# Kernel tuning notes

Measured on AMD Instinct MI355X. Metric: run time of the kernel, lower is better.

The kernel has to match this reference:

```python
import jax, jax.numpy as jnp
import numpy as np

N_HEADS = 16
D_MODEL = 1024
HEAD_DIM = D_MODEL // N_HEADS
MASK_FILL = -1e8  # matches torch masked_fill value -100000000.0


def setup_inputs() -> dict:
    key = jax.random.key(0)
    ks = jax.random.split(key, 12)
    B, L, P = 2, 2048, 2048
    s = 1.0 / np.sqrt(D_MODEL).astype(np.float32)
    inp = {
        "q": jax.random.normal(ks[0], (B, L, D_MODEL), dtype=jnp.float32),
        "k": jax.random.normal(ks[1], (B, P, D_MODEL), dtype=jnp.float32),
        "v": jax.random.normal(ks[2], (B, P, D_MODEL), dtype=jnp.float32),
        "attention_mask": jnp.ones((B, P), dtype=bool),
        "Wq": jax.random.normal(ks[3], (D_MODEL, D_MODEL), dtype=jnp.float32) * s,
        "bq": jnp.zeros((D_MODEL,), dtype=jnp.float32),
        "Wk": jax.random.normal(ks[4], (D_MODEL, D_MODEL), dtype=jnp.float32) * s,
        "bk": jnp.zeros((D_MODEL,), dtype=jnp.float32),
        "Wv": jax.random.normal(ks[5], (D_MODEL, D_MODEL), dtype=jnp.float32) * s,
        "bv": jnp.zeros((D_MODEL,), dtype=jnp.float32),
        "Wo": jax.random.normal(ks[6], (D_MODEL, D_MODEL), dtype=jnp.float32) * s,
        "bo": jnp.zeros((D_MODEL,), dtype=jnp.float32),
    }
    return inp


def _split_heads(x):
    # [B, S, D] -> [B, n, S, h]
    B, S, _ = x.shape
    return x.reshape(B, S, N_HEADS, HEAD_DIM).transpose(0, 2, 1, 3)


def reference(q, k, v, attention_mask, Wq, bq, Wk, bk, Wv, bv, Wo, bo):
    # Linear projections (torch Linear: x @ W.T + b)
    qm = _split_heads(q @ Wq.T + bq)
    km = _split_heads(k @ Wk.T + bk)
    vm = _split_heads(v @ Wv.T + bv)
    # scores: [B, n, L, P]
    scores = jnp.einsum('bnlh,bnph->bnlp', qm, km) / np.sqrt(HEAD_DIM).astype(np.float32)
    # mask [B, P] -> [B, 1, 1, P]; fill False positions with -1e8 (as in torch source)
    mask = attention_mask[:, None, None, :]
    scores = jnp.where(mask, scores, MASK_FILL)
    attn = jax.nn.softmax(scores, axis=-1)
    # dropout is identity in eval mode
    out = jnp.einsum('bnlp,bnph->bnlh', attn, vm)
    B, _, L, _ = out.shape
    out = out.transpose(0, 2, 1, 3).reshape(B, L, D_MODEL)
    return out @ Wo.T + bo
```

## Files before the change

kernel.cpp:

```cpp
#include <hip/hip_runtime.h>
#include <hip/hip_bf16.h>

typedef __attribute__((ext_vector_type(8))) __bf16 bf16x8;
typedef __attribute__((ext_vector_type(4))) float f32x4;
typedef __attribute__((ext_vector_type(16))) float f32x16;
typedef __attribute__((ext_vector_type(4))) unsigned short u16x4;
typedef __attribute__((ext_vector_type(2))) unsigned int u32x2;

#define LOG2E 1.4426950408889634f
#define FIXED_MAX 32.0f

__device__ __forceinline__ unsigned short f2bf(float f) {
  union { float f; unsigned int u; } x;
  x.f = f;
  unsigned int u = x.u;
  u += 0x7fffu + ((u >> 16) & 1u);
  return (unsigned short)(u >> 16);
}

__device__ __forceinline__ float fexp2(float x) {
  float r;
  asm("v_exp_f32 %0, %1" : "=v"(r) : "v"(x));
  return r;
}

__device__ __forceinline__ unsigned int cvtpk_bf16(float lo, float hi) {
  unsigned int r;
  asm("v_cvt_pk_bf16_f32 %0, %1, %2" : "=v"(r) : "v"(lo), "v"(hi));
  return r;
}

__device__ __forceinline__ void plswap(unsigned int& a, unsigned int& b) {
  auto r = __builtin_amdgcn_permlane32_swap((int)a, (int)b, false, false);
  a = (unsigned int)r[0];
  b = (unsigned int)r[1];
}

__device__ __forceinline__ void gload_lds16(const void* gsrc, void* lds) {
  __builtin_amdgcn_global_load_lds(
      (const __attribute__((address_space(1))) unsigned int*)gsrc,
      (__attribute__((address_space(3))) unsigned int*)lds, 16, 0, 0);
}

__global__ __launch_bounds__(256) void cvt_all(
    const float* __restrict__ q, const float* __restrict__ k, const float* __restrict__ v,
    const float* __restrict__ w0, const float* __restrict__ w1,
    const float* __restrict__ w2, const float* __restrict__ w3,
    unsigned short* __restrict__ qb, unsigned short* __restrict__ kb,
    unsigned short* __restrict__ vb, unsigned short* __restrict__ w0b,
    unsigned short* __restrict__ w1b, unsigned short* __restrict__ w2b,
    unsigned short* __restrict__ w3b) {
  long idx = (long)blockIdx.x * 256 + threadIdx.x;
  const long QV = 1024L * 1024;
  const long WQ = 256L * 1024;
  const float* src;
  unsigned short* dst;
  long base;
  if (idx < QV)                { src = q;  dst = qb;  base = idx; }
  else if (idx < 2 * QV)       { src = k;  dst = kb;  base = idx - QV; }
  else if (idx < 3 * QV)       { src = v;  dst = vb;  base = idx - 2 * QV; }
  else if (idx < 3 * QV + WQ)  { src = w0; dst = w0b; base = idx - 3 * QV; }
  else if (idx < 3 * QV + 2*WQ){ src = w1; dst = w1b; base = idx - 3 * QV - WQ; }
  else if (idx < 3 * QV + 3*WQ){ src = w2; dst = w2b; base = idx - 3 * QV - 2 * WQ; }
  else                         { src = w3; dst = w3b; base = idx - 3 * QV - 3 * WQ; }
  f32x4 val = *(const f32x4*)(src + base * 4);
  u16x4 o;
#pragma unroll
  for (int i = 0; i < 4; ++i) o[i] = f2bf(val[i]);
  *(u16x4*)(dst + base * 4) = o;
}

template <int MODE>
__global__ __launch_bounds__(256) void gemm_bt(
    const unsigned short* A0, const unsigned short* A1, const unsigned short* A2,
    const unsigned short* W0, const unsigned short* W1, const unsigned short* W2,
    const float* b0, const float* b1, const float* b2,
    void* o0, void* o1, void* o2) {
  __shared__ char smem[32768];
  constexpr int BM = (MODE == 1) ? 64 : 128;
  constexpr int NF = (MODE == 1) ? 2 : 4;
  const int z = blockIdx.z;
  const unsigned short* __restrict__ A = (z == 0) ? A0 : (z == 1) ? A1 : A2;
  const unsigned short* __restrict__ W = (z == 0) ? W0 : (z == 1) ? W1 : W2;
  const float* __restrict__ bias = (z == 0) ? b0 : (z == 1) ? b1 : b2;
  void* __restrict__ out = (z == 0) ? o0 : (z == 1) ? o1 : o2;
  const float oscale = (MODE == 0 && z == 0) ? 0.125f * LOG2E : 1.0f;

  const int tid = threadIdx.x;
  const int lane = tid & 63;
  const int wave = tid >> 6;
  const int wm = (MODE == 1) ? 0 : (wave >> 1) * 64;
  const int wn = (MODE == 1) ? wave * 32 : (wave & 1) * 64;
  const int bm0 = blockIdx.x * BM;
  const int bn0 = blockIdx.y * 128;
  const int K = 1024;
  const int srow = tid >> 2;
  const int sg = tid & 3;

  f32x4 acc[4][NF] = {};

  auto stageA = [&](int kt, int buf) {
    char* dst = smem + buf * 8192;
#pragma unroll
    for (int h = 0; h < BM / 64; ++h) {
      int row = srow + h * 64;
      int gs = sg ^ ((row >> 1) & 3);
      gload_lds16((const char*)(A + (long)(bm0 + row) * K + kt * 32) + gs * 16,
                  dst + h * 4096 + tid * 16);
    }
  };
  auto stageB = [&](int kt, int buf) {
    char* dst = smem + 16384 + buf * 8192;
#pragma unroll
    for (int h = 0; h < 2; ++h) {
      int row = srow + h * 64;
      int gs = sg ^ ((row >> 1) & 3);
      gload_lds16((const char*)(W + (long)(bn0 + row) * K + kt * 32) + gs * 16,
                  dst + h * 4096 + tid * 16);
    }
  };

  stageA(0, 0);
  stageB(0, 0);
  __syncthreads();

  const int nk = K / 32;
  for (int kt = 0; kt < nk; ++kt) {
    const int cur = kt & 1;
    if (kt + 1 < nk) { stageA(kt + 1, cur ^ 1); stageB(kt + 1, cur ^ 1); }
    char* curA = smem + cur * 8192;
    char* curB = smem + 16384 + cur * 8192;
    const int kb = (lane >> 4) * 16;
    bf16x8 af[4], bfr[NF];
#pragma unroll
    for (int i = 0; i < 4; ++i) {
      int row = wm + i * 16 + (lane & 15);
      af[i] = *(const bf16x8*)(curA + row * 64 + (kb ^ (((row >> 1) & 3) << 4)));
    }
#pragma unroll
    for (int j = 0; j < NF; ++j) {
      int row = wn + j * 16 + (lane & 15);
      bfr[j] = *(const bf16x8*)(curB + row * 64 + (kb ^ (((row >> 1) & 3) << 4)));
    }
#pragma unroll
    for (int i = 0; i < 4; ++i)
#pragma unroll
      for (int j = 0; j < NF; ++j)
        acc[i][j] = __builtin_amdgcn_mfma_f32_16x16x32_bf16(af[i], bfr[j], acc[i][j], 0, 0, 0);
    __syncthreads();
  }

#pragma unroll
  for (int i = 0; i < 4; ++i) {
#pragma unroll
    for (int j = 0; j < NF; ++j) {
#pragma unroll
      for (int r = 0; r < 4; ++r) {
        int row = bm0 + wm + i * 16 + (lane >> 4) * 4 + r;
        int col = bn0 + wn + j * 16 + (lane & 15);
        float vv = (acc[i][j][r] + bias[col]) * oscale;
        if (MODE == 0) {
          int bb = row >> 11, ll = row & 2047;
          int hh = col >> 6, hd = col & 63;
          long idx;
          if (z == 1) {
            idx = ((((long)((bb * 16 + hh) * 32 + (ll >> 6))) * 8 + (hd >> 3)) * 64
                   + (ll & 63)) * 8 + (hd & 7);
          } else if (z == 2) {
            idx = ((((long)((bb * 16 + hh) * 32 + (ll >> 6))) * 8 + ((ll >> 3) & 7)) * 64
                   + hd) * 8 + (ll & 7);
          } else {
            idx = (((long)(bb * 16 + hh) * 2048 + ll) << 6) + hd;
          }
          ((unsigned short*)out)[idx] = f2bf(vv);
        } else {
          ((float*)out)[(long)row * 1024 + col] = vv;
        }
      }
    }
  }
}

__global__ __launch_bounds__(256, 4) void attn_fwd(
    const unsigned short* __restrict__ Qm,
    const unsigned short* __restrict__ Kblk,
    const unsigned short* __restrict__ Vblk,
    const int* __restrict__ mask,
    unsigned short* __restrict__ ao) {
  __shared__ char smem[37504];
  char* const Kl = smem;
  char* const Vl = smem + 16384;
  unsigned short* const maskb = (unsigned short*)(smem + 32768);
  float* const lsums = (float*)(smem + 36864);
  int* const allm = (int*)(smem + 37376);

  const int tid = threadIdx.x, lane = tid & 63, wave = tid >> 6;
  const int kv = wave & 1;
  const int qg = wave >> 1;
  const int h2 = lane >> 5;
  const int ql = lane & 31;
  const int orig = blockIdx.y * 32 + blockIdx.x;
  const int wgid = (orig & 7) * 128 + (orig >> 3);
  const int bh = wgid >> 5, b = bh >> 4, hh = bh & 15;
  const int q0 = (wgid & 31) * 64;
  const unsigned short* Qbase = Qm + ((long)bh * 2048 + q0 + qg * 32) * 64;
  const char* Kg = (const char*)(Kblk + (long)bh * 2048 * 64);
  const char* Vg = (const char*)(Vblk + (long)bh * 2048 * 64);

  auto stage_pair = [&](int s) {
#pragma unroll
    for (int c = 0; c < 4; ++c) {
      int off = (c * 256 + tid) * 16;
      gload_lds16(Kg + (long)s * 16384 + off, Kl + off);
      gload_lds16(Vg + (long)s * 16384 + off, Vl + off);
    }
  };

  stage_pair(0);

  {
    const int* mrow = mask + b * 2048;
    int p8 = tid * 8;
    int ok = 1;
#pragma unroll
    for (int i = 0; i < 4; ++i) {
      int m0 = mrow[p8 + 2 * i];
      int m1 = mrow[p8 + 2 * i + 1];
      ok &= (m0 != 0) & (m1 != 0);
      unsigned int lo = m0 ? 0u : 1u;
      unsigned int hi = m1 ? 0u : 1u;
      *(unsigned int*)(maskb + p8 + 2 * i) = lo | (hi << 16);
    }
    unsigned long long bal = __ballot(ok != 0);
    if (lane < 8) allm[wave * 8 + lane] = (int)(((bal >> (lane * 8)) & 0xFFull) == 0xFFull);
  }

  bf16x8 qf[4];
#pragma unroll
  for (int ks = 0; ks < 4; ++ks)
    qf[ks] = *(const bf16x8*)(Qbase + (long)ql * 64 + ks * 16 + h2 * 8);

  f32x16 o0 = {}, o1 = {};
  float lsum = 0.f;
  const char* const Kc = Kl + kv * 8192;
  const char* const Vc = Vl + kv * 8192;
  __syncthreads();

  for (int s = 0; s < 16; ++s) {
    const int pt = 2 * s + kv;

    f32x16 s0 = {}, s1 = {};
#pragma unroll
    for (int ks = 0; ks < 4; ++ks) {
      int gl = ks * 2 + h2;
      bf16x8 k0 = *(const bf16x8*)(Kc + gl * 1024 + ql * 16);
      bf16x8 k1 = *(const bf16x8*)(Kc + gl * 1024 + 512 + ql * 16);
      s0 = __builtin_amdgcn_mfma_f32_32x32x16_bf16(k0, qf[ks], s0, 0, 0, 0);
      s1 = __builtin_amdgcn_mfma_f32_32x32x16_bf16(k1, qf[ks], s1, 0, 0, 0);
    }

    if (!allm[pt]) {
#pragma unroll
      for (int rq = 0; rq < 4; ++rq) {
        u16x4 m0 = *(const u16x4*)(maskb + pt * 64 + rq * 8 + 4 * h2);
        u16x4 m1 = *(const u16x4*)(maskb + pt * 64 + 32 + rq * 8 + 4 * h2);
#pragma unroll
        for (int i = 0; i < 4; ++i) {
          s0[rq * 4 + i] = m0[i] ? -1.0e8f : s0[rq * 4 + i];
          s1[rq * 4 + i] = m1[i] ? -1.0e8f : s1[rq * 4 + i];
        }
      }
    }

#pragma unroll
    for (int i = 0; i < 16; ++i) {
      float p = fexp2(s0[i] - FIXED_MAX);
      s0[i] = p; lsum += p;
    }
#pragma unroll
    for (int i = 0; i < 16; ++i) {
      float p = fexp2(s1[i] - FIXED_MAX);
      s1[i] = p; lsum += p;
    }

    bf16x8 pa[4];
    {
      union { unsigned int w[4]; bf16x8 v; } u;
      unsigned int w0, w1, w2, w3;
      w0 = cvtpk_bf16(s0[0],  s0[1]);  w1 = cvtpk_bf16(s0[2],  s0[3]);
      w2 = cvtpk_bf16(s0[4],  s0[5]);  w3 = cvtpk_bf16(s0[6],  s0[7]);
      plswap(w0, w2); plswap(w1, w3);
      u.w[0] = w0; u.w[1] = w1; u.w[2] = w2; u.w[3] = w3; pa[0] = u.v;
      w0 = cvtpk_bf16(s0[8],  s0[9]);  w1 = cvtpk_bf16(s0[10], s0[11]);
      w2 = cvtpk_bf16(s0[12], s0[13]); w3 = cvtpk_bf16(s0[14], s0[15]);
      plswap(w0, w2); plswap(w1, w3);
      u.w[0] = w0; u.w[1] = w1; u.w[2] = w2; u.w[3] = w3; pa[1] = u.v;
      w0 = cvtpk_bf16(s1[0],  s1[1]);  w1 = cvtpk_bf16(s1[2],  s1[3]);
      w2 = cvtpk_bf16(s1[4],  s1[5]);  w3 = cvtpk_bf16(s1[6],  s1[7]);
      plswap(w0, w2); plswap(w1, w3);
      u.w[0] = w0; u.w[1] = w1; u.w[2] = w2; u.w[3] = w3; pa[2] = u.v;
      w0 = cvtpk_bf16(s1[8],  s1[9]);  w1 = cvtpk_bf16(s1[10], s1[11]);
      w2 = cvtpk_bf16(s1[12], s1[13]); w3 = cvtpk_bf16(s1[14], s1[15]);
      plswap(w0, w2); plswap(w1, w3);
      u.w[0] = w0; u.w[1] = w1; u.w[2] = w2; u.w[3] = w3; pa[3] = u.v;
    }

#pragma unroll
    for (int kb = 0; kb < 4; ++kb) {
      int gl = kb * 2 + h2;
      bf16x8 v0 = *(const bf16x8*)(Vc + gl * 1024 + ql * 16);
      bf16x8 v1 = *(const bf16x8*)(Vc + gl * 1024 + 512 + ql * 16);
      o0 = __builtin_amdgcn_mfma_f32_32x32x16_bf16(v0, pa[kb], o0, 0, 0, 0);
      o1 = __builtin_amdgcn_mfma_f32_32x32x16_bf16(v1, pa[kb], o1, 0, 0, 0);
    }

    __syncthreads();
    if (s + 1 < 16) {
      stage_pair(s + 1);
      __syncthreads();
    }
  }

  float lf = lsum + __shfl_xor(lsum, 32);
  if (kv == 1) {
    char* Oc = smem + qg * 16384;
#pragma unroll
    for (int rq = 0; rq < 4; ++rq) {
      f32x4 w0 = {o0[rq*4+0], o0[rq*4+1], o0[rq*4+2], o0[rq*4+3]};
      int d4 = (rq * 8 + 4 * h2) * 4;
      *(f32x4*)(Oc + ql * 256 + (d4 ^ ((ql & 7) << 5))) = w0;
      f32x4 w1 = {o1[rq*4+0], o1[rq*4+1], o1[rq*4+2], o1[rq*4+3]};
      int d41 = 128 + d4;
      *(f32x4*)(Oc + ql * 256 + (d41 ^ ((ql & 7) << 5))) = w1;
    }
    if (h2 == 0) lsums[qg * 64 + ql] = lf;
  }
  __syncthreads();
  if (kv == 0) {
    const char* Oc = smem + qg * 16384;
#pragma unroll
    for (int rq = 0; rq < 4; ++rq) {
      int d4 = (rq * 8 + 4 * h2) * 4;
      f32x4 w0 = *(const f32x4*)(Oc + ql * 256 + (d4 ^ ((ql & 7) << 5)));
      f32x4 w1 = *(const f32x4*)(Oc + ql * 256 + ((128 + d4) ^ ((ql & 7) << 5)));
#pragma unroll
      for (int i = 0; i < 4; ++i) { o0[rq*4+i] += w0[i]; o1[rq*4+i] += w1[i]; }
    }
    lf += lsums[qg * 64 + ql];
    float inv = 1.0f / lf;
    unsigned short* aop = ao + ((long)(b * 2048 + q0 + qg * 32 + ql) << 10) + hh * 64;
#pragma unroll
    for (int rq = 0; rq < 4; ++rq) {
      unsigned int lo = cvtpk_bf16(o0[rq * 4 + 0] * inv, o0[rq * 4 + 1] * inv);
      unsigned int hi = cvtpk_bf16(o0[rq * 4 + 2] * inv, o0[rq * 4 + 3] * inv);
      u32x2 st = {lo, hi};
      *(u32x2*)(aop + rq * 8 + 4 * h2) = st;
    }
#pragma unroll
    for (int rq = 0; rq < 4; ++rq) {
      unsigned int lo = cvtpk_bf16(o1[rq * 4 + 0] * inv, o1[rq * 4 + 1] * inv);
      unsigned int hi = cvtpk_bf16(o1[rq * 4 + 2] * inv, o1[rq * 4 + 3] * inv);
      u32x2 st = {lo, hi};
      *(u32x2*)(aop + 32 + rq * 8 + 4 * h2) = st;
    }
  }
}

extern "C" void kernel_launch(void* const* d_in, const int* in_sizes, int n_in,
                              void* d_out, int out_size, void* d_ws, size_t ws_size,
                              hipStream_t stream) {
  const float* q = (const float*)d_in[0];
  const float* k = (const float*)d_in[1];
  const float* v = (const float*)d_in[2];
  const int* mask = (const int*)d_in[3];
  const float* Wq = (const float*)d_in[4];
  const float* bq = (const float*)d_in[5];
  const float* Wk = (const float*)d_in[6];
  const float* bk = (const float*)d_in[7];
  const float* Wv = (const float*)d_in[8];
  const float* bv = (const float*)d_in[9];
  const float* Wo = (const float*)d_in[10];
  const float* bo = (const float*)d_in[11];

  char* ws = (char*)d_ws;
  unsigned short* qb  = (unsigned short*)(ws + (0L << 20));
  unsigned short* kb  = (unsigned short*)(ws + (8L << 20));
  unsigned short* vb  = (unsigned short*)(ws + (16L << 20));
  unsigned short* wqb = (unsigned short*)(ws + (24L << 20));
  unsigned short* wkb = (unsigned short*)(ws + (26L << 20));
  unsigned short* wvb = (unsigned short*)(ws + (28L << 20));
  unsigned short* wob = (unsigned short*)(ws + (30L << 20));
  unsigned short* Qh  = (unsigned short*)(ws + (32L << 20));
  unsigned short* Kb  = (unsigned short*)(ws + (40L << 20));
  unsigned short* Vb  = (unsigned short*)(ws + (56L << 20));
  unsigned short* aob = (unsigned short*)(ws + (64L << 20));

  cvt_all<<<16384, 256, 0, stream>>>(q, k, v, Wq, Wk, Wv, Wo,
                                     qb, kb, vb, wqb, wkb, wvb, wob);
  gemm_bt<0><<<dim3(32, 8, 3), 256, 0, stream>>>(qb, kb, vb, wqb, wkb, wvb,
                                                 bq, bk, bv, Qh, Kb, Vb);
  attn_fwd<<<dim3(32, 32), 256, 0, stream>>>(Qh, Kb, Vb, mask, aob);
  gemm_bt<1><<<dim3(64, 8, 1), 256, 0, stream>>>(aob, aob, aob, wob, wob, wob,
                                                 bo, bo, bo, d_out, d_out, d_out);
  (void)in_sizes; (void)n_in; (void)out_size; (void)ws_size;
}
```

Measured before the change: 126.7 us.

## Fuse fp32-to-bf16 activation conversion into QKV projection GEMM loads

Activations q, k and v are no longer converted to bf16 in a separate pass. The QKV GEMM now streams fp32 tiles straight into LDS with an 8-way XOR swizzle and packs them to bf16 in registers just before the MFMA. This removes a full read and write of three 8 MB fp32 tensors plus the bf16 re-read. The cost is doubled LDS footprint for the A tile (48 KB shared), which may lower occupancy, and more LDS read traffic and conversion instructions inside the inner loop.

```diff
diff --git a/kernel.cpp b/kernel.cpp
--- a/kernel.cpp
+++ b/kernel.cpp
@@ -30,6 +30,15 @@
   return r;
 }
 
+__device__ __forceinline__ bf16x8 pack8(f32x4 a, f32x4 b) {
+  union { unsigned int w[4]; bf16x8 v; } u;
+  u.w[0] = cvtpk_bf16(a[0], a[1]);
+  u.w[1] = cvtpk_bf16(a[2], a[3]);
+  u.w[2] = cvtpk_bf16(b[0], b[1]);
+  u.w[3] = cvtpk_bf16(b[2], b[3]);
+  return u.v;
+}
+
 __device__ __forceinline__ void plswap(unsigned int& a, unsigned int& b) {
   auto r = __builtin_amdgcn_permlane32_swap((int)a, (int)b, false, false);
   a = (unsigned int)r[0];
@@ -42,27 +51,20 @@
       (__attribute__((address_space(3))) unsigned int*)lds, 16, 0, 0);
 }
 
-__global__ __launch_bounds__(256) void cvt_all(
-    const float* __restrict__ q, const float* __restrict__ k, const float* __restrict__ v,
+__global__ __launch_bounds__(256) void cvt_w(
     const float* __restrict__ w0, const float* __restrict__ w1,
     const float* __restrict__ w2, const float* __restrict__ w3,
-    unsigned short* __restrict__ qb, unsigned short* __restrict__ kb,
-    unsigned short* __restrict__ vb, unsigned short* __restrict__ w0b,
-    unsigned short* __restrict__ w1b, unsigned short* __restrict__ w2b,
-    unsigned short* __restrict__ w3b) {
+    unsigned short* __restrict__ w0b, unsigned short* __restrict__ w1b,
+    unsigned short* __restrict__ w2b, unsigned short* __restrict__ w3b) {
   long idx = (long)blockIdx.x * 256 + threadIdx.x;
-  const long QV = 1024L * 1024;
   const long WQ = 256L * 1024;
   const float* src;
   unsigned short* dst;
   long base;
-  if (idx < QV)                { src = q;  dst = qb;  base = idx; }
-  else if (idx < 2 * QV)       { src = k;  dst = kb;  base = idx - QV; }
-  else if (idx < 3 * QV)       { src = v;  dst = vb;  base = idx - 2 * QV; }
-  else if (idx < 3 * QV + WQ)  { src = w0; dst = w0b; base = idx - 3 * QV; }
-  else if (idx < 3 * QV + 2*WQ){ src = w1; dst = w1b; base = idx - 3 * QV - WQ; }
-  else if (idx < 3 * QV + 3*WQ){ src = w2; dst = w2b; base = idx - 3 * QV - 2 * WQ; }
-  else                         { src = w3; dst = w3b; base = idx - 3 * QV - 3 * WQ; }
+  if (idx < WQ)            { src = w0; dst = w0b; base = idx; }
+  else if (idx < 2 * WQ)   { src = w1; dst = w1b; base = idx - WQ; }
+  else if (idx < 3 * WQ)   { src = w2; dst = w2b; base = idx - 2 * WQ; }
+  else                     { src = w3; dst = w3b; base = idx - 3 * WQ; }
   f32x4 val = *(const f32x4*)(src + base * 4);
   u16x4 o;
 #pragma unroll
@@ -72,15 +74,18 @@
 
 template <int MODE>
 __global__ __launch_bounds__(256) void gemm_bt(
-    const unsigned short* A0, const unsigned short* A1, const unsigned short* A2,
+    const void* A0v, const void* A1v, const void* A2v,
     const unsigned short* W0, const unsigned short* W1, const unsigned short* W2,
     const float* b0, const float* b1, const float* b2,
     void* o0, void* o1, void* o2) {
-  __shared__ char smem[32768];
   constexpr int BM = (MODE == 1) ? 64 : 128;
   constexpr int NF = (MODE == 1) ? 2 : 4;
+  constexpr int ABUF = (MODE == 0) ? 16384 : 8192;
+  constexpr int BBASE = (MODE == 0) ? 32768 : 16384;
+  __shared__ char smem[(MODE == 0) ? 49152 : 32768];
   const int z = blockIdx.z;
-  const unsigned short* __restrict__ A = (z == 0) ? A0 : (z == 1) ? A1 : A2;
+  const char* __restrict__ A =
+      (const char*)((z == 0) ? A0v : (z == 1) ? A1v : A2v);
   const unsigned short* __restrict__ W = (z == 0) ? W0 : (z == 1) ? W1 : W2;
   const float* __restrict__ bias = (z == 0) ? b0 : (z == 1) ? b1 : b2;
   void* __restrict__ out = (z == 0) ? o0 : (z == 1) ? o1 : o2;
@@ -100,17 +105,25 @@
   f32x4 acc[4][NF] = {};
 
   auto stageA = [&](int kt, int buf) {
-    char* dst = smem + buf * 8192;
-#pragma unroll
-    for (int h = 0; h < BM / 64; ++h) {
-      int row = srow + h * 64;
+    char* dst = smem + buf * ABUF;
+    if constexpr (MODE == 0) {
+#pragma unroll
+      for (int c = 0; c < 4; ++c) {
+        int slot = c * 256 + tid;
+        int row = slot >> 3, g = slot & 7;
+        int gs = g ^ (row & 7);
+        gload_lds16(A + ((long)(bm0 + row) * K + kt * 32) * 4 + gs * 16,
+                    dst + slot * 16);
+      }
+    } else {
+      int row = srow;
       int gs = sg ^ ((row >> 1) & 3);
-      gload_lds16((const char*)(A + (long)(bm0 + row) * K + kt * 32) + gs * 16,
-                  dst + h * 4096 + tid * 16);
+      gload_lds16(A + ((long)(bm0 + row) * K + kt * 32) * 2 + gs * 16,
+                  dst + tid * 16);
     }
   };
   auto stageB = [&](int kt, int buf) {
-    char* dst = smem + 16384 + buf * 8192;
+    char* dst = smem + BBASE + buf * 8192;
 #pragma unroll
     for (int h = 0; h < 2; ++h) {
       int row = srow + h * 64;
@@ -128,14 +141,26 @@
   for (int kt = 0; kt < nk; ++kt) {
     const int cur = kt & 1;
     if (kt + 1 < nk) { stageA(kt + 1, cur ^ 1); stageB(kt + 1, cur ^ 1); }
-    char* curA = smem + cur * 8192;
-    char* curB = smem + 16384 + cur * 8192;
+    char* curA = smem + cur * ABUF;
+    char* curB = smem + BBASE + cur * 8192;
     const int kb = (lane >> 4) * 16;
     bf16x8 af[4], bfr[NF];
-#pragma unroll
-    for (int i = 0; i < 4; ++i) {
-      int row = wm + i * 16 + (lane & 15);
-      af[i] = *(const bf16x8*)(curA + row * 64 + (kb ^ (((row >> 1) & 3) << 4)));
+    if constexpr (MODE == 0) {
+      const int j0 = (lane >> 4) * 2;
+#pragma unroll
+      for (int i = 0; i < 4; ++i) {
+        int row = wm + i * 16 + (lane & 15);
+        const char* base = curA + row * 128;
+        f32x4 a0 = *(const f32x4*)(base + ((j0 ^ (row & 7)) << 4));
+        f32x4 a1 = *(const f32x4*)(base + (((j0 + 1) ^ (row & 7)) << 4));
+        af[i] = pack8(a0, a1);
+      }
+    } else {
+#pragma unroll
+      for (int i = 0; i < 4; ++i) {
+        int row = wm + i * 16 + (lane & 15);
+        af[i] = *(const bf16x8*)(curA + row * 64 + (kb ^ (((row >> 1) & 3) << 4)));
+      }
     }
 #pragma unroll
     for (int j = 0; j < NF; ++j) {
@@ -383,9 +408,6 @@
   const float* bo = (const float*)d_in[11];
 
   char* ws = (char*)d_ws;
-  unsigned short* qb  = (unsigned short*)(ws + (0L << 20));
-  unsigned short* kb  = (unsigned short*)(ws + (8L << 20));
-  unsigned short* vb  = (unsigned short*)(ws + (16L << 20));
   unsigned short* wqb = (unsigned short*)(ws + (24L << 20));
   unsigned short* wkb = (unsigned short*)(ws + (26L << 20));
   unsigned short* wvb = (unsigned short*)(ws + (28L << 20));
@@ -395,9 +417,8 @@
   unsigned short* Vb  = (unsigned short*)(ws + (56L << 20));
   unsigned short* aob = (unsigned short*)(ws + (64L << 20));
 
-  cvt_all<<<16384, 256, 0, stream>>>(q, k, v, Wq, Wk, Wv, Wo,
-                                     qb, kb, vb, wqb, wkb, wvb, wob);
-  gemm_bt<0><<<dim3(32, 8, 3), 256, 0, stream>>>(qb, kb, vb, wqb, wkb, wvb,
+  cvt_w<<<4096, 256, 0, stream>>>(Wq, Wk, Wv, Wo, wqb, wkb, wvb, wob);
+  gemm_bt<0><<<dim3(32, 8, 3), 256, 0, stream>>>(q, k, v, wqb, wkb, wvb,
                                                  bq, bk, bv, Qh, Kb, Vb);
   attn_fwd<<<dim3(32, 32), 256, 0, stream>>>(Qh, Kb, Vb, mask, aob);
   gemm_bt<1><<<dim3(64, 8, 1), 256, 0, stream>>>(aob, aob, aob, wob, wob, wob,
```

Result: faster. 124.2 us (-2.0%).
